# Kernel tuning notes

Hardware: AMD Instinct MI355X
Metric: run time of the kernel (lower is better)

Reference implementation:

```python
import jax, jax.numpy as jnp
import numpy as np

TEMPERATURE = 0.07
N, D = 16384, 128
NUM_CLASSES = 100


def setup_inputs() -> dict:
    key = jax.random.key(0)
    kf, kl = jax.random.split(key)
    features = jax.random.normal(kf, (N, D), dtype=jnp.float32)
    labels = jax.random.randint(kl, (N,), 0, NUM_CLASSES, dtype=jnp.int64)
    return {"features": features, "labels": labels}


def reference(features, labels):
    # L2-normalize along feature dim (torch F.normalize, eps=1e-12)
    norm = jnp.linalg.norm(features, axis=1, keepdims=True)
    feats = features / jnp.maximum(norm, 1e-12)
    # [N, N] cosine similarity scaled by temperature
    sim = jnp.matmul(feats, feats.T) / TEMPERATURE
    # positive mask: same label, diagonal zeroed
    lab = labels.reshape(-1, 1)
    mask = (lab == lab.T).astype(sim.dtype)
    n = sim.shape[0]
    mask = mask * (1.0 - jnp.eye(n, dtype=sim.dtype))
    exp_sim = jnp.exp(sim)
    # denominator uses (1 - mask): all non-positive pairs INCLUDING the diagonal
    denom = jnp.sum(exp_sim * (1.0 - mask), axis=1)
    numer = jnp.sum(exp_sim * mask, axis=1)
    loss = -jnp.log(numer / denom + 1e-08)
    return jnp.mean(loss)
```

## Files before the change

### kernel.cpp

```cpp
#include <hip/hip_runtime.h>
#include <hip/hip_bf16.h>
#include <cstdint>
#include <cstddef>


#define N_ROWS 16384
#define DIM    128
#define TILE   128
#define NTILES (N_ROWS / TILE)
#define NCHUNK 32

#define FEAT_SCALE 4.5398164f

typedef __attribute__((ext_vector_type(8))) short bf16x8;
typedef __attribute__((ext_vector_type(4))) float f32x4;

typedef const __attribute__((address_space(1))) unsigned int* gas_ptr;
typedef __attribute__((address_space(3))) unsigned int* las_ptr;

__global__ __launch_bounds__(256) void k_normalize(const float* __restrict__ F,
                                                   __hip_bfloat16* __restrict__ G) {
    int tid  = threadIdx.x;
    int lane = tid & 63;
    int wave = tid >> 6;
    int row  = blockIdx.x * 4 + wave;
    const float2* src = (const float2*)(F + (size_t)row * DIM) + lane;
    float2 x = *src;
    float s = x.x * x.x + x.y * x.y;
#pragma unroll
    for (int i = 1; i < 64; i <<= 1) s += __shfl_xor(s, i, 64);
    float scale = FEAT_SCALE / fmaxf(sqrtf(s), 1e-12f);
    __hip_bfloat162 h;
    h.x = __float2bfloat16(x.x * scale);
    h.y = __float2bfloat16(x.y * scale);
    ((__hip_bfloat162*)(G + (size_t)row * DIM))[lane] = h;
}

template<bool ATOM>
__global__ __launch_bounds__(256) void k_tiles(const __hip_bfloat16* __restrict__ G,
                                               const int* __restrict__ lab,
                                               float2* __restrict__ pRow,
                                               float2* __restrict__ pCol) {
    __shared__ __align__(16) char lds[65536 + 2048];
    float* sRed = (float*)(lds + 65536);

    int tid = threadIdx.x;

    int bid = blockIdx.x;
    int u = bid >> 2, i2 = bid & 3;
    int c = (int)((sqrtf(8.f * (float)u + 1.f) - 1.f) * 0.5f);
    while ((c + 1) * (c + 2) / 2 <= u) ++c;
    while (c * (c + 1) / 2 > u) --c;
    int g = u - c * (c + 1) / 2;
    int I = g * 4 + i2;
    int J0 = (I > c * 4) ? I : c * 4;
    int nj = c * 4 + 4 - J0;

    const char* gbase = (const char*)G;
    {
        const char* gA = gbase + (size_t)I * (TILE * DIM * 2);
        const char* gB = gbase + (size_t)J0 * (TILE * DIM * 2);
#pragma unroll
        for (int p = 0; p < 8; ++p) {
            int o = p * 4096 + tid * 16;
            int so = o ^ (((o >> 8) & 7) << 4);
            __builtin_amdgcn_global_load_lds((gas_ptr)(gA + so), (las_ptr)(lds + o), 16, 0, 0);
            __builtin_amdgcn_global_load_lds((gas_ptr)(gB + so), (las_ptr)(lds + 32768 + o), 16, 0, 0);
        }
    }

    int lane = tid & 63, w = tid >> 6;
    int wr = w >> 1, wc = w & 1;
    int lr = lane & 15, lhi = lane >> 4;

    __syncthreads();

    bf16x8 afr[4][4];
#pragma unroll
    for (int m = 0; m < 4; ++m) {
        int row = wr * 64 + m * 16 + lr;
#pragma unroll
        for (int kk = 0; kk < 4; ++kk) {
            int lin = row * 256 + kk * 64 + lhi * 16;
            afr[m][kk] = *(const bf16x8*)(lds + (lin ^ ((row & 7) << 4)));
        }
    }
    int rowbase = I * TILE + wr * 64;
    int labr[4][4];
#pragma unroll
    for (int m = 0; m < 4; ++m)
#pragma unroll
        for (int r = 0; r < 4; ++r) labr[m][r] = lab[rowbase + m * 16 + lhi * 4 + r];

    float rn[4][4], rt[4][4];
#pragma unroll
    for (int m = 0; m < 4; ++m)
#pragma unroll
        for (int r = 0; r < 4; ++r) { rn[m][r] = 0.f; rt[m][r] = 0.f; }

    __syncthreads();

    for (int t = 0; t < nj; ++t) {
        char* buf = lds + (((t & 1) ^ 1) << 15);
        int Jt = J0 + t;

        if (t + 1 < nj) {
            const char* gB = gbase + (size_t)(Jt + 1) * (TILE * DIM * 2);
            char* nbuf = lds + ((t & 1) << 15);
#pragma unroll
            for (int p = 0; p < 8; ++p) {
                int o = p * 4096 + tid * 16;
                int so = o ^ (((o >> 8) & 7) << 4);
                __builtin_amdgcn_global_load_lds((gas_ptr)(gB + so), (las_ptr)(nbuf + o), 16, 0, 0);
            }
        }
        __builtin_amdgcn_sched_barrier(0);

        int colbase = Jt * TILE + wc * 64;
        int labc[4];
#pragma unroll
        for (int n = 0; n < 4; ++n) labc[n] = lab[colbase + n * 16 + lr];

        f32x4 acc[4][4];
#pragma unroll
        for (int m = 0; m < 4; ++m)
#pragma unroll
            for (int n = 0; n < 4; ++n) acc[m][n] = (f32x4){0.f, 0.f, 0.f, 0.f};

#pragma unroll
        for (int kk = 0; kk < 4; ++kk) {
#pragma unroll
            for (int n = 0; n < 4; ++n) {
                int row = wc * 64 + n * 16 + lr;
                int lin = row * 256 + kk * 64 + lhi * 16;
                bf16x8 b = *(const bf16x8*)(buf + (lin ^ ((row & 7) << 4)));
#pragma unroll
                for (int m = 0; m < 4; ++m)
                    acc[m][n] = __builtin_amdgcn_mfma_f32_16x16x32_bf16(afr[m][kk], b, acc[m][n], 0, 0, 0);
            }
        }

        float cn[4] = {0.f, 0.f, 0.f, 0.f}, ct[4] = {0.f, 0.f, 0.f, 0.f};
        bool isdiag = (Jt == I);
        if (isdiag) {
#pragma unroll
            for (int n = 0; n < 4; ++n) {
                int col = colbase + n * 16 + lr;
#pragma unroll
                for (int m = 0; m < 4; ++m) {
                    int row0 = rowbase + m * 16 + lhi * 4;
#pragma unroll
                    for (int r = 0; r < 4; ++r) {
                        float e = __builtin_amdgcn_exp2f(acc[m][n][r]);
                        float te = ((row0 + r) != col) ? e : 0.f;
                        float me = (labr[m][r] == labc[n]) ? te : 0.f;
                        rn[m][r] += me;  rt[m][r] += te;
                        cn[n]    += me;  ct[n]    += te;
                    }
                }
            }
        } else {
#pragma unroll
            for (int n = 0; n < 4; ++n) {
#pragma unroll
                for (int m = 0; m < 4; ++m) {
#pragma unroll
                    for (int r = 0; r < 4; ++r) {
                        float e = __builtin_amdgcn_exp2f(acc[m][n][r]);
                        float me = (labr[m][r] == labc[n]) ? e : 0.f;
                        rn[m][r] += me;  rt[m][r] += e;
                        cn[n]    += me;  ct[n]    += e;
                    }
                }
            }
        }

#pragma unroll
        for (int n = 0; n < 4; ++n) {
            float v1 = cn[n], v2 = ct[n];
            v1 += __shfl_xor(v1, 16, 64); v1 += __shfl_xor(v1, 32, 64);
            v2 += __shfl_xor(v2, 16, 64); v2 += __shfl_xor(v2, 32, 64);
            if (lhi == 0) {
                int colt = wc * 64 + n * 16 + lr;
                sRed[wr * 128 + colt]       = v1;
                sRed[256 + wr * 128 + colt] = v2;
            }
        }
        __syncthreads();
        if (!isdiag && tid < 128) {
            float2 v;
            v.x = sRed[tid] + sRed[128 + tid];
            v.y = sRed[256 + tid] + sRed[384 + tid];
            if (ATOM) {
                float* rN = (float*)pRow;  float* rT = (float*)pCol;
                atomicAdd(&rN[Jt * TILE + tid], v.x);
                atomicAdd(&rT[Jt * TILE + tid], v.y);
            } else {
                pCol[(size_t)I * N_ROWS + Jt * TILE + tid] = v;
            }
        }
        __syncthreads();
    }

#pragma unroll
    for (int m = 0; m < 4; ++m)
#pragma unroll
        for (int r = 0; r < 4; ++r) {
            float v1 = rn[m][r], v2 = rt[m][r];
#pragma unroll
            for (int s = 1; s < 16; s <<= 1) {
                v1 += __shfl_xor(v1, s, 64);
                v2 += __shfl_xor(v2, s, 64);
            }
            if (lr == 0) {
                int rowt = wr * 64 + m * 16 + lhi * 4 + r;
                sRed[wc * 128 + rowt]       = v1;
                sRed[256 + wc * 128 + rowt] = v2;
            }
        }
    __syncthreads();
    if (tid < 128) {
        float2 v;
        v.x = sRed[tid] + sRed[128 + tid];
        v.y = sRed[256 + tid] + sRed[384 + tid];
        if (ATOM) {
            float* rN = (float*)pRow;  float* rT = (float*)pCol;
            atomicAdd(&rN[I * TILE + tid], v.x);
            atomicAdd(&rT[I * TILE + tid], v.y);
        } else {
            pRow[(size_t)c * N_ROWS + I * TILE + tid] = v;
        }
    }
}

template<bool ATOM>
__global__ __launch_bounds__(256) void k_reduce(const float2* __restrict__ pRow,
                                                const float2* __restrict__ pCol,
                                                float* __restrict__ accum) {
    int row = blockIdx.x * 256 + threadIdx.x;
    float num = 0.f, tot = 0.f;
    if (ATOM) {
        num = ((const float*)pRow)[row];
        tot = ((const float*)pCol)[row];
    } else {
        int it = row >> 7;
        for (int c = it >> 2; c < NCHUNK; ++c) {
            float2 v = pRow[(size_t)c * N_ROWS + row];
            num += v.x; tot += v.y;
        }
        for (int I = 0; I < it; ++I) {
            float2 v = pCol[(size_t)I * N_ROWS + row];
            num += v.x; tot += v.y;
        }
    }
    float ediag = expf(14.285714285714286f);
    float denom = tot - num + ediag;
    float loss = -logf(num / denom + 1e-8f);
#pragma unroll
    for (int i = 1; i < 64; i <<= 1) loss += __shfl_xor(loss, i, 64);
    __shared__ float red[4];
    if ((threadIdx.x & 63) == 0) red[threadIdx.x >> 6] = loss;
    __syncthreads();
    if (threadIdx.x == 0)
        atomicAdd(accum, red[0] + red[1] + red[2] + red[3]);
}

__global__ void k_final(const float* __restrict__ accum, float* __restrict__ out) {
    out[0] = accum[0] / (float)N_ROWS;
}

extern "C" void kernel_launch(void* const* d_in, const int* in_sizes, int n_in,
                              void* d_out, int out_size, void* d_ws, size_t ws_size,
                              hipStream_t stream) {
    const float* F  = (const float*)d_in[0];
    const int* lab  = (const int*)d_in[1];
    float* out      = (float*)d_out;
    char* ws        = (char*)d_ws;

    __hip_bfloat16* G = (__hip_bfloat16*)ws;
    float* accum = (float*)(ws + ((size_t)4 << 20));
    char* base   = ws + ((size_t)4 << 20) + 1024;
    float2* pRow = (float2*)base;
    float2* pCol = (float2*)(base + ((size_t)4 << 20));

    k_normalize<<<N_ROWS / 4, 256, 0, stream>>>(F, G);
    hipMemsetAsync(accum, 0, 16, stream);

    size_t need = ((size_t)4 << 20) + 1024 + ((size_t)4 << 20) + ((size_t)16 << 20);
    int nblocks = 2112;
    if (ws_size >= need) {
        k_tiles<false><<<nblocks, 256, 0, stream>>>(G, lab, pRow, pCol);
        k_reduce<false><<<N_ROWS / 256, 256, 0, stream>>>(pRow, pCol, accum);
    } else {
        hipMemsetAsync(pRow, 0, (size_t)N_ROWS * sizeof(float), stream);
        hipMemsetAsync(pCol, 0, (size_t)N_ROWS * sizeof(float), stream);
        k_tiles<true><<<nblocks, 256, 0, stream>>>(G, lab, pRow, pCol);
        k_reduce<true><<<N_ROWS / 256, 256, 0, stream>>>(pRow, pCol, accum);
    }
    k_final<<<1, 1, 0, stream>>>(accum, out);
}
```

Before: 234.7 us.

## Defer per-tile column reductions to end of block and simplify diagonal handling

The tile loop is fully unrolled to at most four column tiles, and per-tile column sums are kept in registers (cnA/ctA) instead of being reduced through shared memory with two barriers every iteration. After the loop, one wave row writes its column partials to LDS and the other adds them and emits pCol or atomics once. The diagonal tile now runs the common exp path and subtracts the self-similarity term afterwards, removing the separate masked branch. This cuts per-iteration barriers and LDS traffic but adds 32 live registers per thread and recomputes one exp per diagonal element, which could lower occupancy.

```diff
diff --git a/kernel.cpp b/kernel.cpp
--- a/kernel.cpp
+++ b/kernel.cpp
@@ -41,7 +41,8 @@
                                                const int* __restrict__ lab,
                                                float2* __restrict__ pRow,
                                                float2* __restrict__ pCol) {
-    __shared__ __align__(16) char lds[65536 + 2048];
+    __shared__ __align__(16) char lds[65536 + 4096];
+    float* sCol = (float*)(lds + 65536);
     float* sRed = (float*)(lds + 65536);
 
     int tid = threadIdx.x;
@@ -86,6 +87,7 @@
         }
     }
     int rowbase = I * TILE + wr * 64;
+    int colwave = wc * 64;
     int labr[4][4];
 #pragma unroll
     for (int m = 0; m < 4; ++m)
@@ -93,73 +95,60 @@
         for (int r = 0; r < 4; ++r) labr[m][r] = lab[rowbase + m * 16 + lhi * 4 + r];
 
     float rn[4][4], rt[4][4];
+    float cnA[4][4], ctA[4][4];
 #pragma unroll
     for (int m = 0; m < 4; ++m)
 #pragma unroll
         for (int r = 0; r < 4; ++r) { rn[m][r] = 0.f; rt[m][r] = 0.f; }
-
-    __syncthreads();
-
-    for (int t = 0; t < nj; ++t) {
-        char* buf = lds + (((t & 1) ^ 1) << 15);
-        int Jt = J0 + t;
-
-        if (t + 1 < nj) {
-            const char* gB = gbase + (size_t)(Jt + 1) * (TILE * DIM * 2);
-            char* nbuf = lds + ((t & 1) << 15);
-#pragma unroll
-            for (int p = 0; p < 8; ++p) {
-                int o = p * 4096 + tid * 16;
-                int so = o ^ (((o >> 8) & 7) << 4);
-                __builtin_amdgcn_global_load_lds((gas_ptr)(gB + so), (las_ptr)(nbuf + o), 16, 0, 0);
-            }
-        }
-        __builtin_amdgcn_sched_barrier(0);
-
-        int colbase = Jt * TILE + wc * 64;
-        int labc[4];
-#pragma unroll
-        for (int n = 0; n < 4; ++n) labc[n] = lab[colbase + n * 16 + lr];
-
-        f32x4 acc[4][4];
-#pragma unroll
-        for (int m = 0; m < 4; ++m)
-#pragma unroll
-            for (int n = 0; n < 4; ++n) acc[m][n] = (f32x4){0.f, 0.f, 0.f, 0.f};
-
-#pragma unroll
-        for (int kk = 0; kk < 4; ++kk) {
-#pragma unroll
-            for (int n = 0; n < 4; ++n) {
-                int row = wc * 64 + n * 16 + lr;
-                int lin = row * 256 + kk * 64 + lhi * 16;
-                bf16x8 b = *(const bf16x8*)(buf + (lin ^ ((row & 7) << 4)));
-#pragma unroll
-                for (int m = 0; m < 4; ++m)
-                    acc[m][n] = __builtin_amdgcn_mfma_f32_16x16x32_bf16(afr[m][kk], b, acc[m][n], 0, 0, 0);
-            }
-        }
-
-        float cn[4] = {0.f, 0.f, 0.f, 0.f}, ct[4] = {0.f, 0.f, 0.f, 0.f};
-        bool isdiag = (Jt == I);
-        if (isdiag) {
-#pragma unroll
-            for (int n = 0; n < 4; ++n) {
-                int col = colbase + n * 16 + lr;
-#pragma unroll
-                for (int m = 0; m < 4; ++m) {
-                    int row0 = rowbase + m * 16 + lhi * 4;
-#pragma unroll
-                    for (int r = 0; r < 4; ++r) {
-                        float e = __builtin_amdgcn_exp2f(acc[m][n][r]);
-                        float te = ((row0 + r) != col) ? e : 0.f;
-                        float me = (labr[m][r] == labc[n]) ? te : 0.f;
-                        rn[m][r] += me;  rt[m][r] += te;
-                        cn[n]    += me;  ct[n]    += te;
-                    }
-                }
-            }
-        } else {
+#pragma unroll
+    for (int t = 0; t < 4; ++t)
+#pragma unroll
+        for (int n = 0; n < 4; ++n) { cnA[t][n] = 0.f; ctA[t][n] = 0.f; }
+
+    __syncthreads();
+
+#pragma unroll
+    for (int t = 0; t < 4; ++t) {
+        if (t < nj) {
+            char* buf = lds + (((t & 1) ^ 1) << 15);
+            int Jt = J0 + t;
+
+            if (t + 1 < nj) {
+                const char* gB = gbase + (size_t)(Jt + 1) * (TILE * DIM * 2);
+                char* nbuf = lds + ((t & 1) << 15);
+#pragma unroll
+                for (int p = 0; p < 8; ++p) {
+                    int o = p * 4096 + tid * 16;
+                    int so = o ^ (((o >> 8) & 7) << 4);
+                    __builtin_amdgcn_global_load_lds((gas_ptr)(gB + so), (las_ptr)(nbuf + o), 16, 0, 0);
+                }
+            }
+            __builtin_amdgcn_sched_barrier(0);
+
+            int colbase = Jt * TILE + colwave;
+            int labc[4];
+#pragma unroll
+            for (int n = 0; n < 4; ++n) labc[n] = lab[colbase + n * 16 + lr];
+
+            f32x4 acc[4][4];
+#pragma unroll
+            for (int m = 0; m < 4; ++m)
+#pragma unroll
+                for (int n = 0; n < 4; ++n) acc[m][n] = (f32x4){0.f, 0.f, 0.f, 0.f};
+
+#pragma unroll
+            for (int kk = 0; kk < 4; ++kk) {
+#pragma unroll
+                for (int n = 0; n < 4; ++n) {
+                    int row = colwave + n * 16 + lr;
+                    int lin = row * 256 + kk * 64 + lhi * 16;
+                    bf16x8 b = *(const bf16x8*)(buf + (lin ^ ((row & 7) << 4)));
+#pragma unroll
+                    for (int m = 0; m < 4; ++m)
+                        acc[m][n] = __builtin_amdgcn_mfma_f32_16x16x32_bf16(afr[m][kk], b, acc[m][n], 0, 0, 0);
+                }
+            }
+
 #pragma unroll
             for (int n = 0; n < 4; ++n) {
 #pragma unroll
@@ -169,38 +158,75 @@
                         float e = __builtin_amdgcn_exp2f(acc[m][n][r]);
                         float me = (labr[m][r] == labc[n]) ? e : 0.f;
                         rn[m][r] += me;  rt[m][r] += e;
-                        cn[n]    += me;  ct[n]    += e;
+                        cnA[t][n] += me; ctA[t][n] += e;
                     }
                 }
             }
-        }
-
-#pragma unroll
-        for (int n = 0; n < 4; ++n) {
-            float v1 = cn[n], v2 = ct[n];
-            v1 += __shfl_xor(v1, 16, 64); v1 += __shfl_xor(v1, 32, 64);
-            v2 += __shfl_xor(v2, 16, 64); v2 += __shfl_xor(v2, 32, 64);
-            if (lhi == 0) {
-                int colt = wc * 64 + n * 16 + lr;
-                sRed[wr * 128 + colt]       = v1;
-                sRed[256 + wr * 128 + colt] = v2;
-            }
-        }
-        __syncthreads();
-        if (!isdiag && tid < 128) {
-            float2 v;
-            v.x = sRed[tid] + sRed[128 + tid];
-            v.y = sRed[256 + tid] + sRed[384 + tid];
-            if (ATOM) {
-                float* rN = (float*)pRow;  float* rT = (float*)pCol;
-                atomicAdd(&rN[Jt * TILE + tid], v.x);
-                atomicAdd(&rT[Jt * TILE + tid], v.y);
-            } else {
-                pCol[(size_t)I * N_ROWS + Jt * TILE + tid] = v;
-            }
-        }
-        __syncthreads();
-    }
+
+            if (Jt == I) {
+#pragma unroll
+                for (int m = 0; m < 4; ++m)
+#pragma unroll
+                    for (int r = 0; r < 4; ++r) {
+                        bool d = (wr == wc) && (lhi * 4 + r == lr);
+                        float e = __builtin_amdgcn_exp2f(acc[m][m][r]);
+                        e = d ? e : 0.f;
+                        rn[m][r] -= e;  rt[m][r] -= e;
+                        cnA[t][m] -= e; ctA[t][m] -= e;
+                    }
+            }
+
+            __syncthreads();
+        }
+    }
+
+    if (wr == 0) {
+#pragma unroll
+        for (int t = 0; t < 4; ++t)
+#pragma unroll
+            for (int n = 0; n < 4; ++n) {
+                float v1 = cnA[t][n], v2 = ctA[t][n];
+                v1 += __shfl_xor(v1, 16, 64); v1 += __shfl_xor(v1, 32, 64);
+                v2 += __shfl_xor(v2, 16, 64); v2 += __shfl_xor(v2, 32, 64);
+                if (lhi == 0) {
+                    int idx = ((wc * 4 + t) * 4 + n) * 16 + lr;
+                    sCol[idx]       = v1;
+                    sCol[512 + idx] = v2;
+                }
+            }
+    }
+    __syncthreads();
+    if (wr == 1) {
+#pragma unroll
+        for (int t = 0; t < 4; ++t) {
+            if (t < nj) {
+                int Jt = J0 + t;
+                if (Jt != I) {
+#pragma unroll
+                    for (int n = 0; n < 4; ++n) {
+                        float v1 = cnA[t][n], v2 = ctA[t][n];
+                        v1 += __shfl_xor(v1, 16, 64); v1 += __shfl_xor(v1, 32, 64);
+                        v2 += __shfl_xor(v2, 16, 64); v2 += __shfl_xor(v2, 32, 64);
+                        if (lhi == 0) {
+                            int idx = ((wc * 4 + t) * 4 + n) * 16 + lr;
+                            v1 += sCol[idx];
+                            v2 += sCol[512 + idx];
+                            int col = colwave + n * 16 + lr;
+                            if (ATOM) {
+                                float* rNd = (float*)pRow;  float* rTd = (float*)pCol;
+                                atomicAdd(&rNd[Jt * TILE + col], v1);
+                                atomicAdd(&rTd[Jt * TILE + col], v2);
+                            } else {
+                                float2 v; v.x = v1; v.y = v2;
+                                pCol[(size_t)I * N_ROWS + Jt * TILE + col] = v;
+                            }
+                        }
+                    }
+                }
+            }
+        }
+    }
+    __syncthreads();
 
 #pragma unroll
     for (int m = 0; m < 4; ++m)
@@ -224,9 +250,9 @@
         v.x = sRed[tid] + sRed[128 + tid];
         v.y = sRed[256 + tid] + sRed[384 + tid];
         if (ATOM) {
-            float* rN = (float*)pRow;  float* rT = (float*)pCol;
-            atomicAdd(&rN[I * TILE + tid], v.x);
-            atomicAdd(&rT[I * TILE + tid], v.y);
+            float* rNd = (float*)pRow;  float* rTd = (float*)pCol;
+            atomicAdd(&rNd[I * TILE + tid], v.x);
+            atomicAdd(&rTd[I * TILE + tid], v.y);
         } else {
             pRow[(size_t)c * N_ROWS + I * TILE + tid] = v;
         }
```

Result: faster. 229.6 us (-2.1%).
